# Optimization experiments

Hardware: AMD Instinct MI355X
Metric: run time of the kernel (lower is better)

## Reference

```python
import jax, jax.numpy as jnp
import numpy as np

B, C, H, W = 512, 1, 280, 280
K, S, F = 28, 28, 10           # kernel, stride, nfilters
HS, WS = 10, 10                # output spatial spans (280/28)
SPAN = HS * WS                 # 100 patch locations
OUT = 10                       # out_channels
DEC_IN = HS * WS * F           # 1000


def setup_inputs() -> dict:
    key = jax.random.key(0)
    k1, k2, k3, k4, k5 = jax.random.split(key, 5)
    x = jax.random.normal(k1, (B, C, H, W), dtype=jnp.float32)
    # locally-connected weights: one kernel per (filter, spatial location), torch layout [F*SPAN, C, K, K]
    conv_w = jax.random.normal(k2, (F * SPAN, C, K, K), dtype=jnp.float32) * 0.02
    conv_b = jax.random.normal(k3, (F * SPAN, C), dtype=jnp.float32) * 0.02
    dec_w = jax.random.normal(k4, (OUT, DEC_IN), dtype=jnp.float32) * 0.02
    dec_b = jax.random.normal(k5, (OUT,), dtype=jnp.float32) * 0.02
    return {"x": x, "conv_w": conv_w, "conv_b": conv_b, "dec_w": dec_w, "dec_b": dec_b}


def reference(x, conv_w, conv_b, dec_w, dec_b):
    # Extract non-overlapping KxK patches (stride == kernel_size, padding == 0):
    # [B,C,H,W] -> [B,C,HS,K,WS,K] -> [B,HS,WS,C,K,K] -> [B,SPAN,C,K,K]
    # matches torch unfold(2).unfold(3) ordering (height span outer, width span inner).
    patches = x.reshape(B, C, HS, K, WS, K).transpose(0, 2, 4, 1, 3, 5)
    patches = patches.reshape(B, SPAN, C, K, K)
    # weight index in torch is f*SPAN + s (x is tiled SPAN-fastest by repeat)
    w = conv_w.reshape(F, SPAN, C, K, K)
    # per-location elementwise mul + reduce over (kh, kw) == batched tiny contraction
    out = jnp.einsum('bscij,fscij->bfsc', patches, w)  # [B,F,SPAN,C]
    out = out + conv_b.reshape(F, SPAN, C)
    out = out.reshape(B, F, HS, WS)  # valid since C == 1 (as in torch view)
    out = jax.nn.relu(out).reshape(B, DEC_IN)
    return out @ dec_w.T + dec_b
```

## Files before the change

kernel.cpp:

```cpp
#include <hip/hip_runtime.h>
#include <hip/hip_bf16.h>

#define HW      280
#define IMG     78400
#define KK      28
#define F_N     10
#define SPAN    100
#define OUT_N   10
#define P_PLANE 512000

typedef short s16x8 __attribute__((ext_vector_type(8)));
typedef float f32x4 __attribute__((ext_vector_type(4)));

static __device__ __forceinline__ unsigned bits2(__hip_bfloat162 h) {
  return *reinterpret_cast<unsigned*>(&h);
}

#define RAW_BARRIER() asm volatile("s_waitcnt lgkmcnt(0)\ns_barrier" ::: "memory")

__global__ __launch_bounds__(256) void wprep(const float* __restrict__ cw,
                                             uint4* __restrict__ wbuf4) {
  const int idx = blockIdx.x * 256 + (int)threadIdx.x;
  if (idx >= 28000) return;
  const int fs = idx / 28;
  const int r  = idx - fs * 28;
  const int f  = fs / 100;
  const int s  = fs - f * 100;

  const float* src = cw + (size_t)idx * 28;
  float v[28];
#pragma unroll
  for (int j = 0; j < 7; ++j)
    *reinterpret_cast<float4*>(&v[j * 4]) =
        *reinterpret_cast<const float4*>(src + j * 4);

  unsigned p[16];
#pragma unroll
  for (int k2 = 0; k2 < 14; ++k2)
    p[k2] = bits2(__float22bfloat162_rn(make_float2(v[2 * k2], v[2 * k2 + 1])));
  p[14] = 0u; p[15] = 0u;

  uint4* dst = wbuf4 + ((size_t)(s * 28 + r) * 16 + f) * 4;
  dst[0] = make_uint4(p[0],  p[1],  p[2],  p[3]);
  dst[1] = make_uint4(p[4],  p[5],  p[6],  p[7]);
  dst[2] = make_uint4(p[8],  p[9],  p[10], p[11]);
  dst[3] = make_uint4(p[12], p[13], p[14], p[15]);
}

__global__ __launch_bounds__(256, 4) void lcn_conv(
    const float* __restrict__ x, const unsigned short* __restrict__ wbuf,
    float* __restrict__ P) {
  const int bid  = blockIdx.x;
  const int xcd  = bid & 7;
  const int grp  = bid >> 3;
  const int hsrq = xcd + 8 * (grp % 5);
  const int bg   = grp / 5;
  const int hs   = hsrq >> 2;
  const int rq   = hsrq & 3;

  const int tid  = (int)threadIdx.x;
  const int lane = tid & 63;
  const int wid  = tid >> 6;
  const int l15  = lane & 15;
  const int kg   = lane >> 4;

  __shared__ short xl[2][16 * 320];

  for (int i = tid; i < 2 * 160; i += 256) {
    const int buf = i / 160, j = i - buf * 160;
    const int b = j / 10, ws = j - b * 10;
    const int sidx = (b * 320 + ws * 32 + 28) ^ ((b & 7) << 3);
    *reinterpret_cast<short4*>(&xl[buf][sidx]) = make_short4(0, 0, 0, 0);
  }

  const int nun = (wid < 2) ? 3 : 2;
  const int wsl[3] = {wid, wid + 4, wid + 8};

  f32x4 acc[3];
#pragma unroll
  for (int u = 0; u < 3; ++u) acc[u] = (f32x4){0.f, 0.f, 0.f, 0.f};

  const int row0 = hs * KK + rq * 7;
  const float* xbase = x + (size_t)bg * 16 * IMG + (size_t)row0 * HW;

  float4 stgA[5], stgB[5];

#define ISSUE(STG, R)                                                       \
  _Pragma("unroll")                                                         \
  for (int j = 0; j < 5; ++j) {                                             \
    const int i = tid + 256 * j;                                            \
    if (i < 1120) {                                                         \
      const int b = i / 70, q = i - b * 70;                                 \
      STG[j] = *reinterpret_cast<const float4*>(                            \
          xbase + (size_t)b * IMG + (size_t)(R) * HW + q * 4);              \
    }                                                                       \
  }

#define COMMIT(STG, BUF)                                                    \
  _Pragma("unroll")                                                         \
  for (int j = 0; j < 5; ++j) {                                             \
    const int i = tid + 256 * j;                                            \
    if (i < 1120) {                                                         \
      const int b = i / 70, q = i - b * 70;                                 \
      const int ws = q / 7, c4 = q - ws * 7;                                \
      const int sidx = (b * 320 + ws * 32 + c4 * 4) ^ ((b & 7) << 3);       \
      uint2 pk;                                                             \
      pk.x = bits2(__float22bfloat162_rn(make_float2(STG[j].x, STG[j].y))); \
      pk.y = bits2(__float22bfloat162_rn(make_float2(STG[j].z, STG[j].w))); \
      *reinterpret_cast<uint2*>(&xl[BUF][sidx]) = pk;                       \
    }                                                                       \
  }

  ISSUE(stgA, 0)
  ISSUE(stgB, 1)
  COMMIT(stgA, 0)
  RAW_BARRIER();

#pragma unroll
  for (int r = 0; r < 7; ++r) {
    const int buf = r & 1;
    const int rr  = rq * 7 + r;

    s16x8 bfr[3];
#pragma unroll
    for (int u = 0; u < 3; ++u)
      bfr[u] = *reinterpret_cast<const s16x8*>(
          wbuf + (size_t)((hs * 10 + wsl[u]) * 28 + rr) * 512 + l15 * 32 + kg * 8);

    if (r + 2 < 7) {
      if (r & 1) { ISSUE(stgB, r + 2) } else { ISSUE(stgA, r + 2) }
    }

#pragma unroll
    for (int u = 0; u < 3; ++u) {
      if (u < nun) {
        const int ws = wsl[u];
        const int sidx = (l15 * 320 + ws * 32 + kg * 8) ^ ((l15 & 7) << 3);
        const s16x8 afr = *reinterpret_cast<const s16x8*>(&xl[buf][sidx]);
        acc[u] = __builtin_amdgcn_mfma_f32_16x16x32_bf16(afr, bfr[u], acc[u], 0, 0, 0);
      }
    }

    if (r < 6) {
      if (r & 1) { COMMIT(stgA, buf ^ 1) } else { COMMIT(stgB, buf ^ 1) }
      RAW_BARRIER();
    }
  }

  if (l15 < F_N) {
#pragma unroll
    for (int u = 0; u < 3; ++u) {
      if (u < nun) {
        const int s = hs * 10 + wsl[u];
        float* Pp = P + (size_t)rq * P_PLANE + (size_t)(l15 * SPAN + s) * 512
                      + bg * 16 + kg * 4;
        *reinterpret_cast<float4*>(Pp) =
            make_float4(acc[u][0], acc[u][1], acc[u][2], acc[u][3]);
      }
    }
  }
}

__global__ __launch_bounds__(256) void lcn_dec(
    const float* __restrict__ P, const float* __restrict__ cb,
    const float* __restrict__ dw, float* __restrict__ yp) {
  const int dchunk = blockIdx.x >> 3;
  const int bgrp   = blockIdx.x & 7;
  const int tid    = (int)threadIdx.x;
  const int bl     = tid & 63;
  const int dway   = tid >> 6;
  const int b      = bgrp * 64 + bl;

  const float* Pb = P + b;
  float acc[OUT_N];
#pragma unroll
  for (int o = 0; o < OUT_N; ++o) acc[o] = 0.f;

#pragma unroll
  for (int dd = 0; dd < 10; ++dd) {
    const int d = dchunk * 40 + dway * 10 + dd;
    const float* pd = Pb + (size_t)d * 512;
    const float p = pd[0] + pd[P_PLANE] + pd[2 * (size_t)P_PLANE]
                          + pd[3 * (size_t)P_PLANE];
    const float h = fmaxf(p + cb[d], 0.f);
#pragma unroll
    for (int o = 0; o < OUT_N; ++o)
      acc[o] = fmaf(h, dw[o * 1000 + d], acc[o]);
  }

  __shared__ float red[3][OUT_N][64];
  if (dway > 0) {
#pragma unroll
    for (int o = 0; o < OUT_N; ++o) red[dway - 1][o][bl] = acc[o];
  }
  __syncthreads();
  if (dway == 0) {
#pragma unroll
    for (int o = 0; o < OUT_N; ++o) {
      const float v = acc[o] + red[0][o][bl] + red[1][o][bl] + red[2][o][bl];
      yp[(size_t)(dchunk * OUT_N + o) * 512 + b] = v;
    }
  }
}

__global__ __launch_bounds__(256) void lcn_yred(
    const float* __restrict__ yp, const float* __restrict__ db,
    float* __restrict__ y) {
  const int idx = blockIdx.x * 256 + (int)threadIdx.x;
  const int o = idx >> 9;
  const int b = idx & 511;
  float a = db[o];
#pragma unroll
  for (int p = 0; p < 25; ++p) a += yp[(size_t)p * 5120 + idx];
  y[b * OUT_N + o] = a;
}

extern "C" void kernel_launch(void* const* d_in, const int* in_sizes, int n_in,
                              void* d_out, int out_size, void* d_ws, size_t ws_size,
                              hipStream_t stream) {
  const float* x  = (const float*)d_in[0];
  const float* cw = (const float*)d_in[1];
  const float* cb = (const float*)d_in[2];
  const float* dw = (const float*)d_in[3];
  const float* db = (const float*)d_in[4];
  float* y = (float*)d_out;

  float* P  = (float*)d_ws;
  float* yp = P + 4 * (size_t)P_PLANE;
  uint4* wbuf = (uint4*)(yp + 25 * 5120);

  wprep   <<<dim3(110),  dim3(256), 0, stream>>>(cw, wbuf);
  lcn_conv<<<dim3(1280), dim3(256), 0, stream>>>(x, (const unsigned short*)wbuf, P);
  lcn_dec <<<dim3(200),  dim3(256), 0, stream>>>(P, cb, dw, yp);
  lcn_yred<<<dim3(20),   dim3(256), 0, stream>>>(yp, db, y);
}
```

Measured before the change: 43.53 us.

## Fuse bias, ReLU and decoder into conv kernel, one block per full row-span

```diff
diff --git a/kernel.cpp b/kernel.cpp
--- a/kernel.cpp
+++ b/kernel.cpp
@@ -7,7 +7,6 @@
 #define F_N     10
 #define SPAN    100
 #define OUT_N   10
-#define P_PLANE 512000
 
 typedef short s16x8 __attribute__((ext_vector_type(8)));
 typedef float f32x4 __attribute__((ext_vector_type(4)));
@@ -49,14 +48,11 @@
 
 __global__ __launch_bounds__(256, 4) void lcn_conv(
     const float* __restrict__ x, const unsigned short* __restrict__ wbuf,
-    float* __restrict__ P) {
-  const int bid  = blockIdx.x;
-  const int xcd  = bid & 7;
-  const int grp  = bid >> 3;
-  const int hsrq = xcd + 8 * (grp % 5);
-  const int bg   = grp / 5;
-  const int hs   = hsrq >> 2;
-  const int rq   = hsrq & 3;
+    const float* __restrict__ cb, const float* __restrict__ dw,
+    float* __restrict__ yp) {
+  const int bid = blockIdx.x;
+  const int hs  = bid % 10;
+  const int bg  = bid / 10;
 
   const int tid  = (int)threadIdx.x;
   const int lane = tid & 63;
@@ -65,6 +61,14 @@
   const int kg   = lane >> 4;
 
   __shared__ short xl[2][16 * 320];
+  __shared__ float h_lds[100 * 16];
+  __shared__ float dw_lds[1000];
+
+  for (int i = tid; i < 1000; i += 256) {
+    const int o  = i / 100, dl = i - o * 100;
+    const int f  = dl / 10, ws = dl - f * 10;
+    dw_lds[i] = dw[o * 1000 + f * 100 + hs * 10 + ws];
+  }
 
   for (int i = tid; i < 2 * 160; i += 256) {
     const int buf = i / 160, j = i - buf * 160;
@@ -80,8 +84,7 @@
 #pragma unroll
   for (int u = 0; u < 3; ++u) acc[u] = (f32x4){0.f, 0.f, 0.f, 0.f};
 
-  const int row0 = hs * KK + rq * 7;
-  const float* xbase = x + (size_t)bg * 16 * IMG + (size_t)row0 * HW;
+  const float* xbase = x + (size_t)bg * 16 * IMG + (size_t)(hs * KK) * HW;
 
   float4 stgA[5], stgB[5];
 
@@ -111,95 +114,72 @@
     }                                                                       \
   }
 
+#define BLOAD(BFR, RR)                                                      \
+  _Pragma("unroll")                                                         \
+  for (int u = 0; u < 3; ++u)                                               \
+    BFR[u] = *reinterpret_cast<const s16x8*>(                               \
+        wbuf + (size_t)((hs * 10 + wsl[u]) * 28 + (RR)) * 512 + l15 * 32 + kg * 8);
+
+#define MFMAS(BFR, BUF)                                                     \
+  _Pragma("unroll")                                                         \
+  for (int u = 0; u < 3; ++u) {                                             \
+    if (u < nun) {                                                          \
+      const int sidx = (l15 * 320 + wsl[u] * 32 + kg * 8) ^ ((l15 & 7) << 3); \
+      const s16x8 afr = *reinterpret_cast<const s16x8*>(&xl[BUF][sidx]);    \
+      acc[u] = __builtin_amdgcn_mfma_f32_16x16x32_bf16(afr, BFR[u], acc[u], 0, 0, 0); \
+    }                                                                       \
+  }
+
   ISSUE(stgA, 0)
   ISSUE(stgB, 1)
   COMMIT(stgA, 0)
   RAW_BARRIER();
 
-#pragma unroll
-  for (int r = 0; r < 7; ++r) {
-    const int buf = r & 1;
-    const int rr  = rq * 7 + r;
-
-    s16x8 bfr[3];
-#pragma unroll
-    for (int u = 0; u < 3; ++u)
-      bfr[u] = *reinterpret_cast<const s16x8*>(
-          wbuf + (size_t)((hs * 10 + wsl[u]) * 28 + rr) * 512 + l15 * 32 + kg * 8);
-
-    if (r + 2 < 7) {
-      if (r & 1) { ISSUE(stgB, r + 2) } else { ISSUE(stgA, r + 2) }
+#pragma unroll 1
+  for (int r2 = 0; r2 < 14; ++r2) {
+    const int re = 2 * r2;
+    s16x8 bfrE[3];
+    BLOAD(bfrE, re)
+    if (re + 2 < 28) { ISSUE(stgA, re + 2) }
+    MFMAS(bfrE, 0)
+    COMMIT(stgB, 1)
+    RAW_BARRIER();
+    const int ro = re + 1;
+    s16x8 bfrO[3];
+    BLOAD(bfrO, ro)
+    if (ro + 2 < 28) { ISSUE(stgB, ro + 2) }
+    MFMAS(bfrO, 1)
+    if (r2 < 13) {
+      COMMIT(stgA, 0)
+      RAW_BARRIER();
     }
-
+  }
+
+  if (l15 < F_N) {
 #pragma unroll
     for (int u = 0; u < 3; ++u) {
       if (u < nun) {
         const int ws = wsl[u];
-        const int sidx = (l15 * 320 + ws * 32 + kg * 8) ^ ((l15 & 7) << 3);
-        const s16x8 afr = *reinterpret_cast<const s16x8*>(&xl[buf][sidx]);
-        acc[u] = __builtin_amdgcn_mfma_f32_16x16x32_bf16(afr, bfr[u], acc[u], 0, 0, 0);
+        const float bias = cb[l15 * 100 + hs * 10 + ws];
+        float4 hv;
+        hv.x = fmaxf(acc[u][0] + bias, 0.f);
+        hv.y = fmaxf(acc[u][1] + bias, 0.f);
+        hv.z = fmaxf(acc[u][2] + bias, 0.f);
+        hv.w = fmaxf(acc[u][3] + bias, 0.f);
+        *reinterpret_cast<float4*>(&h_lds[(l15 * 10 + ws) * 16 + kg * 4]) = hv;
       }
     }
-
-    if (r < 6) {
-      if (r & 1) { COMMIT(stgA, buf ^ 1) } else { COMMIT(stgB, buf ^ 1) }
-      RAW_BARRIER();
-    }
-  }
-
-  if (l15 < F_N) {
-#pragma unroll
-    for (int u = 0; u < 3; ++u) {
-      if (u < nun) {
-        const int s = hs * 10 + wsl[u];
-        float* Pp = P + (size_t)rq * P_PLANE + (size_t)(l15 * SPAN + s) * 512
-                      + bg * 16 + kg * 4;
-        *reinterpret_cast<float4*>(Pp) =
-            make_float4(acc[u][0], acc[u][1], acc[u][2], acc[u][3]);
-      }
-    }
-  }
-}
-
-__global__ __launch_bounds__(256) void lcn_dec(
-    const float* __restrict__ P, const float* __restrict__ cb,
-    const float* __restrict__ dw, float* __restrict__ yp) {
-  const int dchunk = blockIdx.x >> 3;
-  const int bgrp   = blockIdx.x & 7;
-  const int tid    = (int)threadIdx.x;
-  const int bl     = tid & 63;
-  const int dway   = tid >> 6;
-  const int b      = bgrp * 64 + bl;
-
-  const float* Pb = P + b;
-  float acc[OUT_N];
-#pragma unroll
-  for (int o = 0; o < OUT_N; ++o) acc[o] = 0.f;
-
-#pragma unroll
-  for (int dd = 0; dd < 10; ++dd) {
-    const int d = dchunk * 40 + dway * 10 + dd;
-    const float* pd = Pb + (size_t)d * 512;
-    const float p = pd[0] + pd[P_PLANE] + pd[2 * (size_t)P_PLANE]
-                          + pd[3 * (size_t)P_PLANE];
-    const float h = fmaxf(p + cb[d], 0.f);
-#pragma unroll
-    for (int o = 0; o < OUT_N; ++o)
-      acc[o] = fmaf(h, dw[o * 1000 + d], acc[o]);
-  }
-
-  __shared__ float red[3][OUT_N][64];
-  if (dway > 0) {
-#pragma unroll
-    for (int o = 0; o < OUT_N; ++o) red[dway - 1][o][bl] = acc[o];
   }
   __syncthreads();
-  if (dway == 0) {
-#pragma unroll
-    for (int o = 0; o < OUT_N; ++o) {
-      const float v = acc[o] + red[0][o][bl] + red[1][o][bl] + red[2][o][bl];
-      yp[(size_t)(dchunk * OUT_N + o) * 512 + b] = v;
-    }
+
+  if (tid < 16 * OUT_N) {
+    const int b16 = tid & 15;
+    const int o   = tid >> 4;
+    float a = 0.f;
+#pragma unroll 10
+    for (int dl = 0; dl < 100; ++dl)
+      a = fmaf(h_lds[dl * 16 + b16], dw_lds[o * 100 + dl], a);
+    yp[(size_t)(hs * OUT_N + o) * 512 + bg * 16 + b16] = a;
   }
 }
 
@@ -211,7 +191,8 @@
   const int b = idx & 511;
   float a = db[o];
 #pragma unroll
-  for (int p = 0; p < 25; ++p) a += yp[(size_t)p * 5120 + idx];
+  for (int hs = 0; hs < 10; ++hs)
+    a += yp[(size_t)(hs * OUT_N + o) * 512 + b];
   y[b * OUT_N + o] = a;
 }
 
@@ -225,12 +206,11 @@
   const float* db = (const float*)d_in[4];
   float* y = (float*)d_out;
 
-  float* P  = (float*)d_ws;
-  float* yp = P + 4 * (size_t)P_PLANE;
-  uint4* wbuf = (uint4*)(yp + 25 * 5120);
-
-  wprep   <<<dim3(110),  dim3(256), 0, stream>>>(cw, wbuf);
-  lcn_conv<<<dim3(1280), dim3(256), 0, stream>>>(x, (const unsigned short*)wbuf, P);
-  lcn_dec <<<dim3(200),  dim3(256), 0, stream>>>(P, cb, dw, yp);
-  lcn_yred<<<dim3(20),   dim3(256), 0, stream>>>(yp, db, y);
-}
+  float* yp   = (float*)d_ws;
+  uint4* wbuf = (uint4*)(yp + 100 * 512);
+
+  wprep   <<<dim3(110), dim3(256), 0, stream>>>(cw, wbuf);
+  lcn_conv<<<dim3(320), dim3(256), 0, stream>>>(x, (const unsigned short*)wbuf,
+                                                cb, dw, yp);
+  lcn_yred<<<dim3(20),  dim3(256), 0, stream>>>(yp, db, y);
+}
```

Result: faster. 42.05 us (-3.4%).
